# Optimization experiments

Measured on AMD Instinct MI355X. Metric: run time of the kernel, lower is better.

## Reference

```python
import jax, jax.numpy as jnp
import numpy as np

B, T, H, IN, OUT = 128, 256, 1024, 1, 1


def setup_inputs() -> dict:
    key = jax.random.key(0)
    ks = jax.random.split(key, 11)
    s = 1.0 / np.sqrt(H)
    u = lambda k, shape: jax.random.uniform(k, shape, jnp.float32, -s, s)
    return {
        "input_X": jax.random.normal(ks[0], (B, T), jnp.float32),
        "W_ih0": u(ks[1], (4 * H, IN)),
        "W_hh0": u(ks[2], (4 * H, H)),
        "b_ih0": u(ks[3], (4 * H,)),
        "b_hh0": u(ks[4], (4 * H,)),
        "W_ih1": u(ks[5], (4 * H, H)),
        "W_hh1": u(ks[6], (4 * H, H)),
        "b_ih1": u(ks[7], (4 * H,)),
        "b_hh1": u(ks[8], (4 * H,)),
        "W_lin": u(ks[9], (OUT, H)),
        "b_lin": u(ks[10], (OUT,)),
        "future": 0,
    }


def _lstm_cell(x, h, c, W_ih, W_hh, b_ih, b_hh):
    # gates: [B, 4H], PyTorch LSTMCell gate order: i, f, g, o
    gates = x @ W_ih.T + b_ih + h @ W_hh.T + b_hh
    i, f, g, o = jnp.split(gates, 4, axis=-1)
    c_new = jax.nn.sigmoid(f) * c + jax.nn.sigmoid(i) * jnp.tanh(g)
    h_new = jax.nn.sigmoid(o) * jnp.tanh(c_new)
    return h_new, c_new


def reference(input_X, W_ih0, W_hh0, b_ih0, b_hh0, W_ih1, W_hh1, b_ih1, b_hh1,
              W_lin, b_lin, future):
    batch = input_X.shape[0]
    h0 = jnp.zeros((batch, H), input_X.dtype)
    c0 = jnp.zeros((batch, H), input_X.dtype)
    h1 = jnp.zeros((batch, H), input_X.dtype)
    c1 = jnp.zeros((batch, H), input_X.dtype)

    def step(carry, x_t):  # x_t: [B, 1]
        h0, c0, h1, c1 = carry
        h0, c0 = _lstm_cell(x_t, h0, c0, W_ih0, W_hh0, b_ih0, b_hh0)
        h1, c1 = _lstm_cell(h0, h1, c1, W_ih1, W_hh1, b_ih1, b_hh1)
        y = h1 @ W_lin.T + b_lin  # [B, OUT]
        return (h0, c0, h1, c1), y

    xs = input_X.T[:, :, None]  # [T, B, 1]
    carry, ys = jax.lax.scan(step, (h0, c0, h1, c1), xs)
    outputs = jnp.transpose(ys, (1, 0, 2))  # [B, T, OUT]

    y = ys[-1]
    fut = []
    for _ in range(int(future)):
        carry, y = step(carry, y)
        fut.append(y)
    if fut:
        outputs = jnp.concatenate([outputs, jnp.stack(fut, axis=1)], axis=1)
    return jnp.squeeze(outputs, axis=2)  # [B, T+future]
```

## Files before the change

kernel.cpp:

```cpp
#include <hip/hip_runtime.h>
#include <stdint.h>

typedef _Float16 f16;
typedef f16 half8 __attribute__((ext_vector_type(8)));
typedef float f32x4 __attribute__((ext_vector_type(4)));
typedef unsigned long long u64;

constexpr int HID = 1024;
constexpr int NBAT = 128;
constexpr int SEQ = 256;
constexpr int NL0 = 64;
constexpr int NL1 = 128;
constexpr int NBLK = NL0 + NL1;
constexpr int HROWB = 4096;
constexpr int NSLOT = 258;
constexpr size_t SLOTE = (size_t)NBAT * 2048;
constexpr int WROWB0 = 2064;
constexpr int WROWB1 = 4112;
constexpr int ZOFF = 32 * WROWB1;
constexpr int ZBYTES = 4160;
constexpr int WLDS = ZOFF + ZBYTES;
constexpr int LDS_TOTAL = WLDS + 4096;

constexpr int SY_INIT = 0;
constexpr int SY_BARG = 32;
constexpr int SY_CNT = 64;
constexpr int SY_BARAX = 64 + 256;

__device__ __forceinline__ float sigm(float x) { return 1.0f / (1.0f + __expf(-x)); }
__device__ __forceinline__ float tanh_(float x) {
  float e = __expf(2.0f * x);
  return (e - 1.0f) / (e + 1.0f);
}
__device__ __forceinline__ void vm0() {
  asm volatile("s_waitcnt vmcnt(0)" ::: "memory");
}
__device__ __forceinline__ void push8(void* dst, u64 v) {
  (void)__hip_atomic_exchange((u64*)dst, v, __ATOMIC_RELAXED, __HIP_MEMORY_SCOPE_AGENT);
}
__device__ __forceinline__ void spin_until(int* p, int target) {
  uint64_t t0 = __builtin_amdgcn_s_memtime();
  while (__hip_atomic_load(p, __ATOMIC_RELAXED, __HIP_MEMORY_SCOPE_AGENT) < target) {
    __builtin_amdgcn_s_sleep(1);
    if (__builtin_amdgcn_s_memtime() - t0 > (1ULL << 29)) break;
  }
}

__global__ __launch_bounds__(256, 1) void lstm_persist(
    const float* __restrict__ X,
    const float* __restrict__ Wih0, const float* __restrict__ Whh0,
    const float* __restrict__ bih0, const float* __restrict__ bhh0,
    const float* __restrict__ Wih1, const float* __restrict__ Whh1,
    const float* __restrict__ bih1, const float* __restrict__ bhh1,
    const float* __restrict__ Wlin,
    f16* __restrict__ Hbuf,
    float* __restrict__ yp,
    int* __restrict__ sy) {
  extern __shared__ char smem[];
  char* Wl = smem;
  char* Pk = smem + WLDS;

  const int bid = blockIdx.x, tid = threadIdx.x;
  const bool isL0 = bid < NL0;
  const int j = isL0 ? bid : bid - NL0;
  const int w = tid >> 6, l = tid & 63;
  const int l15 = l & 15, lhi = l >> 4;

  int xcd;
  asm volatile("s_getreg_b32 %0, hwreg(HW_REG_XCC_ID)" : "=s"(xcd));
  xcd &= 7;

  if (isL0) {
    for (int it = 0; it < 256; ++it) {
      int e = it * 256 + tid;
      int r = e >> 10, k = e & 1023;
      int grow = (r >> 4) * HID + j * 16 + (r & 15);
      *(f16*)(Wl + r * WROWB0 + 2 * k) = (f16)Whh0[(size_t)grow * HID + k];
    }
  } else {
    for (int it = 0; it < 256; ++it) {
      int e = it * 256 + tid;
      int r = e >> 11, k = e & 2047;
      int grow = (r >> 3) * HID + j * 8 + (r & 7);
      float v = (k < 1024) ? Wih1[(size_t)grow * HID + k]
                           : Whh1[(size_t)grow * HID + (k - 1024)];
      *(f16*)(Wl + r * WROWB1 + 2 * k) = (f16)v;
    }
    for (int e = tid; e < ZBYTES / 2; e += 256)
      *(f16*)(Wl + ZOFF + 2 * e) = (f16)0.f;
  }

  float bi, bf, bg, bo, wi_i = 0, wi_f = 0, wi_g = 0, wi_o = 0, wl = 0;
  if (isL0) {
    int m = j * 16 + l15;
    bi = bih0[m] + bhh0[m];
    bf = bih0[HID + m] + bhh0[HID + m];
    bg = bih0[2 * HID + m] + bhh0[2 * HID + m];
    bo = bih0[3 * HID + m] + bhh0[3 * HID + m];
    wi_i = Wih0[m]; wi_f = Wih0[HID + m];
    wi_g = Wih0[2 * HID + m]; wi_o = Wih0[3 * HID + m];
  } else {
    int u = j * 8 + (l15 & 7);
    bi = bih1[u] + bhh1[u];
    bf = bih1[HID + u] + bhh1[HID + u];
    bg = bih1[2 * HID + u] + bhh1[2 * HID + u];
    bo = bih1[3 * HID + u] + bhh1[3 * HID + u];
    wl = (l15 < 8) ? Wlin[u] : 0.f;
  }
  float cst[8];
#pragma unroll
  for (int q = 0; q < 8; ++q) cst[q] = 0.f;

  int cx = 0, nx = 0;
  if (tid == 0) {
    __hip_atomic_fetch_add(&sy[SY_CNT + 32 * xcd], 1, __ATOMIC_RELAXED,
                           __HIP_MEMORY_SCOPE_AGENT);
    __hip_atomic_fetch_add(&sy[SY_INIT], 1, __ATOMIC_RELAXED, __HIP_MEMORY_SCOPE_AGENT);
    spin_until(&sy[SY_INIT], NBLK);
    cx = __hip_atomic_load(&sy[SY_CNT + 32 * xcd], __ATOMIC_RELAXED,
                           __HIP_MEMORY_SCOPE_AGENT);
#pragma unroll
    for (int x = 0; x < 8; ++x)
      nx += (__hip_atomic_load(&sy[SY_CNT + 32 * x], __ATOMIC_RELAXED,
                               __HIP_MEMORY_SCOPE_AGENT) > 0);
  }
  __syncthreads();

  const char* Wb = Wl + l15 * WROWB0 + lhi * 16;
  const char* Wg0 = Wl + ((l15 < 8) ? (0 * 8 + l15) * WROWB1 : ZOFF) + lhi * 16;
  const char* Wg1 = Wl + ((l15 < 8) ? (1 * 8 + l15) * WROWB1 : ZOFF) + lhi * 16;
  const char* Wg2 = Wl + ((l15 < 8) ? (2 * 8 + l15) * WROWB1 : ZOFF) + lhi * 16;
  const char* Wg3 = Wl + ((l15 < 8) ? (3 * 8 + l15) * WROWB1 : ZOFF) + lhi * 16;

  for (int i = 1; i <= SEQ + 1; ++i) {
    const bool active = isL0 ? (i <= SEQ) : (i >= 2);
    if (active) {
      const char* Asrc = (const char*)(Hbuf + (size_t)(i - 1) * SLOTE);
      char* Hw = (char*)(Hbuf + (size_t)i * SLOTE);
      const char* a0p = Asrc + (size_t)(32 * w + l15) * HROWB + lhi * 16;
      const char* a1p = a0p + (size_t)16 * HROWB;

      if (isL0) {
        float xr[8];
#pragma unroll
        for (int mf = 0; mf < 2; ++mf)
#pragma unroll
          for (int r = 0; r < 4; ++r)
            xr[mf * 4 + r] = X[(32 * w + 16 * mf + 4 * lhi + r) * SEQ + (i - 1)];

        half8 pa[8], pb[8];
#pragma unroll
        for (int k0 = 0; k0 < 8; ++k0) {
          pa[k0] = *(const half8*)(a0p + k0 * 64);
          pb[k0] = *(const half8*)(a1p + k0 * 64);
        }
        f32x4 acc[2][4];
#pragma unroll
        for (int mf = 0; mf < 2; ++mf)
#pragma unroll
          for (int n = 0; n < 4; ++n) acc[mf][n] = f32x4{0.f, 0.f, 0.f, 0.f};

#pragma unroll
        for (int ck = 0; ck < 32; ++ck) {
          half8 a0 = pa[ck & 7], a1 = pb[ck & 7];
          if (ck < 24) {
            pa[ck & 7] = *(const half8*)(a0p + (ck + 8) * 64);
            pb[ck & 7] = *(const half8*)(a1p + (ck + 8) * 64);
          }
          half8 b0 = *(const half8*)(Wb + ck * 64);
          half8 b1 = *(const half8*)(Wb + 16 * WROWB0 + ck * 64);
          half8 b2 = *(const half8*)(Wb + 32 * WROWB0 + ck * 64);
          half8 b3 = *(const half8*)(Wb + 48 * WROWB0 + ck * 64);
          acc[0][0] = __builtin_amdgcn_mfma_f32_16x16x32_f16(a0, b0, acc[0][0], 0, 0, 0);
          acc[0][1] = __builtin_amdgcn_mfma_f32_16x16x32_f16(a0, b1, acc[0][1], 0, 0, 0);
          acc[0][2] = __builtin_amdgcn_mfma_f32_16x16x32_f16(a0, b2, acc[0][2], 0, 0, 0);
          acc[0][3] = __builtin_amdgcn_mfma_f32_16x16x32_f16(a0, b3, acc[0][3], 0, 0, 0);
          acc[1][0] = __builtin_amdgcn_mfma_f32_16x16x32_f16(a1, b0, acc[1][0], 0, 0, 0);
          acc[1][1] = __builtin_amdgcn_mfma_f32_16x16x32_f16(a1, b1, acc[1][1], 0, 0, 0);
          acc[1][2] = __builtin_amdgcn_mfma_f32_16x16x32_f16(a1, b2, acc[1][2], 0, 0, 0);
          acc[1][3] = __builtin_amdgcn_mfma_f32_16x16x32_f16(a1, b3, acc[1][3], 0, 0, 0);
        }

#pragma unroll
        for (int mf = 0; mf < 2; ++mf) {
#pragma unroll
          for (int r = 0; r < 4; ++r) {
            float xv = xr[mf * 4 + r];
            float gi = acc[mf][0][r] + bi + xv * wi_i;
            float gf = acc[mf][1][r] + bf + xv * wi_f;
            float gg = acc[mf][2][r] + bg + xv * wi_g;
            float go = acc[mf][3][r] + bo + xv * wi_o;
            float cn = sigm(gf) * cst[mf * 4 + r] + sigm(gi) * tanh_(gg);
            float hn = sigm(go) * tanh_(cn);
            cst[mf * 4 + r] = cn;
            *(f16*)(Pk + w * 1024 + (16 * mf + 4 * lhi + r) * 32 + l15 * 2) = (f16)hn;
          }
        }
        asm volatile("s_waitcnt lgkmcnt(0)" ::: "memory");
        {
          const char* src = Pk + w * 1024 + (l >> 1) * 32 + (l & 1) * 16;
          u64 v0 = *(const u64*)src;
          u64 v1 = *(const u64*)(src + 8);
          char* dst = Hw + (size_t)(32 * w + (l >> 1)) * HROWB + j * 32 + (l & 1) * 16;
          push8(dst, v0);
          push8(dst + 8, v1);
        }
      } else {
        half8 pa[8], pb[8];
#pragma unroll
        for (int k0 = 0; k0 < 8; ++k0) {
          pa[k0] = *(const half8*)(a0p + k0 * 64);
          pb[k0] = *(const half8*)(a1p + k0 * 64);
        }
        f32x4 acc[2][4];
#pragma unroll
        for (int mf = 0; mf < 2; ++mf)
#pragma unroll
          for (int n = 0; n < 4; ++n) acc[mf][n] = f32x4{0.f, 0.f, 0.f, 0.f};

#pragma unroll
        for (int ck = 0; ck < 64; ++ck) {
          half8 a0 = pa[ck & 7], a1 = pb[ck & 7];
          if (ck < 56) {
            pa[ck & 7] = *(const half8*)(a0p + (ck + 8) * 64);
            pb[ck & 7] = *(const half8*)(a1p + (ck + 8) * 64);
          }
          half8 b0 = *(const half8*)(Wg0 + ck * 64);
          half8 b1 = *(const half8*)(Wg1 + ck * 64);
          half8 b2 = *(const half8*)(Wg2 + ck * 64);
          half8 b3 = *(const half8*)(Wg3 + ck * 64);
          acc[0][0] = __builtin_amdgcn_mfma_f32_16x16x32_f16(a0, b0, acc[0][0], 0, 0, 0);
          acc[0][1] = __builtin_amdgcn_mfma_f32_16x16x32_f16(a0, b1, acc[0][1], 0, 0, 0);
          acc[0][2] = __builtin_amdgcn_mfma_f32_16x16x32_f16(a0, b2, acc[0][2], 0, 0, 0);
          acc[0][3] = __builtin_amdgcn_mfma_f32_16x16x32_f16(a0, b3, acc[0][3], 0, 0, 0);
          acc[1][0] = __builtin_amdgcn_mfma_f32_16x16x32_f16(a1, b0, acc[1][0], 0, 0, 0);
          acc[1][1] = __builtin_amdgcn_mfma_f32_16x16x32_f16(a1, b1, acc[1][1], 0, 0, 0);
          acc[1][2] = __builtin_amdgcn_mfma_f32_16x16x32_f16(a1, b2, acc[1][2], 0, 0, 0);
          acc[1][3] = __builtin_amdgcn_mfma_f32_16x16x32_f16(a1, b3, acc[1][3], 0, 0, 0);
        }

#pragma unroll
        for (int mf = 0; mf < 2; ++mf) {
#pragma unroll
          for (int r = 0; r < 4; ++r) {
            int b = 32 * w + 16 * mf + 4 * lhi + r;
            float gi = acc[mf][0][r] + bi;
            float gf = acc[mf][1][r] + bf;
            float gg = acc[mf][2][r] + bg;
            float go = acc[mf][3][r] + bo;
            float cn = sigm(gf) * cst[mf * 4 + r] + sigm(gi) * tanh_(gg);
            float hn = sigm(go) * tanh_(cn);
            cst[mf * 4 + r] = cn;
            if (l15 < 8)
              *(f16*)(Pk + w * 512 + (16 * mf + 4 * lhi + r) * 16 + l15 * 2) = (f16)hn;
            float v = hn * wl;
            v += __shfl_xor(v, 1);
            v += __shfl_xor(v, 2);
            v += __shfl_xor(v, 4);
            v += __shfl_xor(v, 8);
            if (l15 == 0)
              yp[(size_t)(i - 2) * NBAT * NL1 + b * NL1 + j] = v;
          }
        }
        asm volatile("s_waitcnt lgkmcnt(0)" ::: "memory");
        {
          u64 v = *(const u64*)(Pk + w * 512 + (l >> 1) * 16 + (l & 1) * 8);
          char* dst =
              Hw + (size_t)(32 * w + (l >> 1)) * HROWB + 2048 + j * 16 + (l & 1) * 8;
          push8(dst, v);
        }
      }
    }

    if (i <= SEQ) {
      vm0();
      __syncthreads();
      if (tid == 0) {
        int old = __hip_atomic_fetch_add(&sy[SY_BARAX + 32 * xcd], 1, __ATOMIC_RELAXED,
                                         __HIP_MEMORY_SCOPE_AGENT);
        if (old == cx * i - 1)
          __hip_atomic_fetch_add(&sy[SY_BARG], 1, __ATOMIC_RELAXED,
                                 __HIP_MEMORY_SCOPE_AGENT);
        spin_until(&sy[SY_BARG], nx * i);
      }
      __syncthreads();
    }
  }
}

__global__ __launch_bounds__(256) void zero_ws(f16* Hbuf, int* sy) {
  int g = blockIdx.x * 256 + threadIdx.x, gs = gridDim.x * 256;
  for (size_t idx = g; idx < 2 * SLOTE; idx += gs) Hbuf[idx] = (f16)0.f;
  for (int idx = g; idx < 1024; idx += gs) sy[idx] = 0;
}

__global__ __launch_bounds__(256) void final_kernel(const float* __restrict__ yp,
                                                    const float* __restrict__ blin,
                                                    float* __restrict__ out) {
  const int idx = blockIdx.x * blockDim.x + threadIdx.x;
  const int t = idx >> 7, b = idx & 127;
  const float* p = yp + ((size_t)t * NBAT + b) * NL1;
  float s = 0.f;
#pragma unroll
  for (int q = 0; q < NL1; ++q) s += p[q];
  out[b * SEQ + t] = s + blin[0];
}

extern "C" void kernel_launch(void* const* d_in, const int* in_sizes, int n_in,
                              void* d_out, int out_size, void* d_ws, size_t ws_size,
                              hipStream_t stream) {
  const float* X = (const float*)d_in[0];
  const float* Wih0 = (const float*)d_in[1];
  const float* Whh0 = (const float*)d_in[2];
  const float* bih0 = (const float*)d_in[3];
  const float* bhh0 = (const float*)d_in[4];
  const float* Wih1 = (const float*)d_in[5];
  const float* Whh1 = (const float*)d_in[6];
  const float* bih1 = (const float*)d_in[7];
  const float* bhh1 = (const float*)d_in[8];
  const float* Wlin = (const float*)d_in[9];
  const float* blin = (const float*)d_in[10];
  float* out = (float*)d_out;

  char* p = (char*)d_ws;
  f16* Hbuf = (f16*)p;    p += (size_t)NSLOT * SLOTE * 2;
  float* yp = (float*)p;  p += (size_t)SEQ * NBAT * NL1 * 4;
  int* sy = (int*)p;      p += 1024 * 4;

  hipFuncSetAttribute((const void*)lstm_persist,
                      hipFuncAttributeMaxDynamicSharedMemorySize, LDS_TOTAL);

  zero_ws<<<256, 256, 0, stream>>>(Hbuf, sy);

  lstm_persist<<<NBLK, 256, LDS_TOTAL, stream>>>(
      X, Wih0, Whh0, bih0, bhh0, Wih1, Whh1, bih1, bhh1, Wlin,
      Hbuf, yp, sy);

  final_kernel<<<NBAT, 256, 0, stream>>>(yp, blin, out);
}
```

Before: 4.890 ms.

## Split grid barrier per layer and double waves per block

After: 4.735 ms. 1.03x faster.

```diff
diff --git a/kernel.cpp b/kernel.cpp
--- a/kernel.cpp
+++ b/kernel.cpp
@@ -23,9 +23,12 @@
 constexpr int LDS_TOTAL = WLDS + 4096;
 
 constexpr int SY_INIT = 0;
-constexpr int SY_BARG = 32;
-constexpr int SY_CNT = 64;
-constexpr int SY_BARAX = 64 + 256;
+constexpr int SY_BG0 = 32;
+constexpr int SY_BG1 = 64;
+constexpr int SY_CNT0 = 96;
+constexpr int SY_CNT1 = 96 + 256;
+constexpr int SY_BARX0 = 96 + 512;
+constexpr int SY_BARX1 = 96 + 768;
 
 __device__ __forceinline__ float sigm(float x) { return 1.0f / (1.0f + __expf(-x)); }
 __device__ __forceinline__ float tanh_(float x) {
@@ -46,7 +49,7 @@
   }
 }
 
-__global__ __launch_bounds__(256, 1) void lstm_persist(
+__global__ __launch_bounds__(512, 1) void lstm_persist(
     const float* __restrict__ X,
     const float* __restrict__ Wih0, const float* __restrict__ Whh0,
     const float* __restrict__ bih0, const float* __restrict__ bhh0,
@@ -71,22 +74,22 @@
   xcd &= 7;
 
   if (isL0) {
-    for (int it = 0; it < 256; ++it) {
-      int e = it * 256 + tid;
+    for (int it = 0; it < 128; ++it) {
+      int e = it * 512 + tid;
       int r = e >> 10, k = e & 1023;
       int grow = (r >> 4) * HID + j * 16 + (r & 15);
       *(f16*)(Wl + r * WROWB0 + 2 * k) = (f16)Whh0[(size_t)grow * HID + k];
     }
   } else {
-    for (int it = 0; it < 256; ++it) {
-      int e = it * 256 + tid;
+    for (int it = 0; it < 128; ++it) {
+      int e = it * 512 + tid;
       int r = e >> 11, k = e & 2047;
       int grow = (r >> 3) * HID + j * 8 + (r & 7);
       float v = (k < 1024) ? Wih1[(size_t)grow * HID + k]
                            : Whh1[(size_t)grow * HID + (k - 1024)];
       *(f16*)(Wl + r * WROWB1 + 2 * k) = (f16)v;
     }
-    for (int e = tid; e < ZBYTES / 2; e += 256)
+    for (int e = tid; e < ZBYTES / 2; e += 512)
       *(f16*)(Wl + ZOFF + 2 * e) = (f16)0.f;
   }
 
@@ -107,22 +110,25 @@
     bo = bih1[3 * HID + u] + bhh1[3 * HID + u];
     wl = (l15 < 8) ? Wlin[u] : 0.f;
   }
-  float cst[8];
-#pragma unroll
-  for (int q = 0; q < 8; ++q) cst[q] = 0.f;
-
-  int cx = 0, nx = 0;
+  float cst[4];
+#pragma unroll
+  for (int q = 0; q < 4; ++q) cst[q] = 0.f;
+
+  int cxm = 0, nx0 = 0, nx1 = 0;
   if (tid == 0) {
-    __hip_atomic_fetch_add(&sy[SY_CNT + 32 * xcd], 1, __ATOMIC_RELAXED,
-                           __HIP_MEMORY_SCOPE_AGENT);
+    __hip_atomic_fetch_add(&sy[(isL0 ? SY_CNT0 : SY_CNT1) + 32 * xcd], 1,
+                           __ATOMIC_RELAXED, __HIP_MEMORY_SCOPE_AGENT);
     __hip_atomic_fetch_add(&sy[SY_INIT], 1, __ATOMIC_RELAXED, __HIP_MEMORY_SCOPE_AGENT);
     spin_until(&sy[SY_INIT], NBLK);
-    cx = __hip_atomic_load(&sy[SY_CNT + 32 * xcd], __ATOMIC_RELAXED,
-                           __HIP_MEMORY_SCOPE_AGENT);
-#pragma unroll
-    for (int x = 0; x < 8; ++x)
-      nx += (__hip_atomic_load(&sy[SY_CNT + 32 * x], __ATOMIC_RELAXED,
-                               __HIP_MEMORY_SCOPE_AGENT) > 0);
+    cxm = __hip_atomic_load(&sy[(isL0 ? SY_CNT0 : SY_CNT1) + 32 * xcd],
+                            __ATOMIC_RELAXED, __HIP_MEMORY_SCOPE_AGENT);
+#pragma unroll
+    for (int x = 0; x < 8; ++x) {
+      nx0 += (__hip_atomic_load(&sy[SY_CNT0 + 32 * x], __ATOMIC_RELAXED,
+                                __HIP_MEMORY_SCOPE_AGENT) > 0);
+      nx1 += (__hip_atomic_load(&sy[SY_CNT1 + 32 * x], __ATOMIC_RELAXED,
+                                __HIP_MEMORY_SCOPE_AGENT) > 0);
+    }
   }
   __syncthreads();
 
@@ -133,140 +139,112 @@
   const char* Wg3 = Wl + ((l15 < 8) ? (3 * 8 + l15) * WROWB1 : ZOFF) + lhi * 16;
 
   for (int i = 1; i <= SEQ + 1; ++i) {
+    if (i >= 2) {
+      if (tid == 0) {
+        spin_until(&sy[SY_BG0], nx0 * (i - 1));
+        if (!isL0) spin_until(&sy[SY_BG1], nx1 * (i - 1));
+      }
+      __syncthreads();
+    }
+
     const bool active = isL0 ? (i <= SEQ) : (i >= 2);
     if (active) {
       const char* Asrc = (const char*)(Hbuf + (size_t)(i - 1) * SLOTE);
       char* Hw = (char*)(Hbuf + (size_t)i * SLOTE);
-      const char* a0p = Asrc + (size_t)(32 * w + l15) * HROWB + lhi * 16;
-      const char* a1p = a0p + (size_t)16 * HROWB;
+      const char* a0p = Asrc + (size_t)(16 * w + l15) * HROWB + lhi * 16;
 
       if (isL0) {
-        float xr[8];
-#pragma unroll
-        for (int mf = 0; mf < 2; ++mf)
-#pragma unroll
-          for (int r = 0; r < 4; ++r)
-            xr[mf * 4 + r] = X[(32 * w + 16 * mf + 4 * lhi + r) * SEQ + (i - 1)];
-
-        half8 pa[8], pb[8];
-#pragma unroll
-        for (int k0 = 0; k0 < 8; ++k0) {
-          pa[k0] = *(const half8*)(a0p + k0 * 64);
-          pb[k0] = *(const half8*)(a1p + k0 * 64);
-        }
-        f32x4 acc[2][4];
-#pragma unroll
-        for (int mf = 0; mf < 2; ++mf)
-#pragma unroll
-          for (int n = 0; n < 4; ++n) acc[mf][n] = f32x4{0.f, 0.f, 0.f, 0.f};
+        float xr[4];
+#pragma unroll
+        for (int r = 0; r < 4; ++r)
+          xr[r] = X[(16 * w + 4 * lhi + r) * SEQ + (i - 1)];
+
+        half8 pa[8];
+#pragma unroll
+        for (int k0 = 0; k0 < 8; ++k0) pa[k0] = *(const half8*)(a0p + k0 * 64);
+        f32x4 acc[4];
+#pragma unroll
+        for (int n = 0; n < 4; ++n) acc[n] = f32x4{0.f, 0.f, 0.f, 0.f};
 
 #pragma unroll
         for (int ck = 0; ck < 32; ++ck) {
-          half8 a0 = pa[ck & 7], a1 = pb[ck & 7];
-          if (ck < 24) {
-            pa[ck & 7] = *(const half8*)(a0p + (ck + 8) * 64);
-            pb[ck & 7] = *(const half8*)(a1p + (ck + 8) * 64);
-          }
+          half8 a0 = pa[ck & 7];
+          if (ck < 24) pa[ck & 7] = *(const half8*)(a0p + (ck + 8) * 64);
           half8 b0 = *(const half8*)(Wb + ck * 64);
           half8 b1 = *(const half8*)(Wb + 16 * WROWB0 + ck * 64);
           half8 b2 = *(const half8*)(Wb + 32 * WROWB0 + ck * 64);
           half8 b3 = *(const half8*)(Wb + 48 * WROWB0 + ck * 64);
-          acc[0][0] = __builtin_amdgcn_mfma_f32_16x16x32_f16(a0, b0, acc[0][0], 0, 0, 0);
-          acc[0][1] = __builtin_amdgcn_mfma_f32_16x16x32_f16(a0, b1, acc[0][1], 0, 0, 0);
-          acc[0][2] = __builtin_amdgcn_mfma_f32_16x16x32_f16(a0, b2, acc[0][2], 0, 0, 0);
-          acc[0][3] = __builtin_amdgcn_mfma_f32_16x16x32_f16(a0, b3, acc[0][3], 0, 0, 0);
-          acc[1][0] = __builtin_amdgcn_mfma_f32_16x16x32_f16(a1, b0, acc[1][0], 0, 0, 0);
-          acc[1][1] = __builtin_amdgcn_mfma_f32_16x16x32_f16(a1, b1, acc[1][1], 0, 0, 0);
-          acc[1][2] = __builtin_amdgcn_mfma_f32_16x16x32_f16(a1, b2, acc[1][2], 0, 0, 0);
-          acc[1][3] = __builtin_amdgcn_mfma_f32_16x16x32_f16(a1, b3, acc[1][3], 0, 0, 0);
-        }
-
-#pragma unroll
-        for (int mf = 0; mf < 2; ++mf) {
-#pragma unroll
-          for (int r = 0; r < 4; ++r) {
-            float xv = xr[mf * 4 + r];
-            float gi = acc[mf][0][r] + bi + xv * wi_i;
-            float gf = acc[mf][1][r] + bf + xv * wi_f;
-            float gg = acc[mf][2][r] + bg + xv * wi_g;
-            float go = acc[mf][3][r] + bo + xv * wi_o;
-            float cn = sigm(gf) * cst[mf * 4 + r] + sigm(gi) * tanh_(gg);
-            float hn = sigm(go) * tanh_(cn);
-            cst[mf * 4 + r] = cn;
-            *(f16*)(Pk + w * 1024 + (16 * mf + 4 * lhi + r) * 32 + l15 * 2) = (f16)hn;
-          }
+          acc[0] = __builtin_amdgcn_mfma_f32_16x16x32_f16(a0, b0, acc[0], 0, 0, 0);
+          acc[1] = __builtin_amdgcn_mfma_f32_16x16x32_f16(a0, b1, acc[1], 0, 0, 0);
+          acc[2] = __builtin_amdgcn_mfma_f32_16x16x32_f16(a0, b2, acc[2], 0, 0, 0);
+          acc[3] = __builtin_amdgcn_mfma_f32_16x16x32_f16(a0, b3, acc[3], 0, 0, 0);
+        }
+
+#pragma unroll
+        for (int r = 0; r < 4; ++r) {
+          float xv = xr[r];
+          float gi = acc[0][r] + bi + xv * wi_i;
+          float gf = acc[1][r] + bf + xv * wi_f;
+          float gg = acc[2][r] + bg + xv * wi_g;
+          float go = acc[3][r] + bo + xv * wi_o;
+          float cn = sigm(gf) * cst[r] + sigm(gi) * tanh_(gg);
+          float hn = sigm(go) * tanh_(cn);
+          cst[r] = cn;
+          *(f16*)(Pk + w * 512 + (4 * lhi + r) * 32 + l15 * 2) = (f16)hn;
         }
         asm volatile("s_waitcnt lgkmcnt(0)" ::: "memory");
         {
-          const char* src = Pk + w * 1024 + (l >> 1) * 32 + (l & 1) * 16;
-          u64 v0 = *(const u64*)src;
-          u64 v1 = *(const u64*)(src + 8);
-          char* dst = Hw + (size_t)(32 * w + (l >> 1)) * HROWB + j * 32 + (l & 1) * 16;
-          push8(dst, v0);
-          push8(dst + 8, v1);
+          u64 v = *(const u64*)(Pk + w * 512 + (l >> 2) * 32 + (l & 3) * 8);
+          char* dst = Hw + (size_t)(16 * w + (l >> 2)) * HROWB + j * 32 + (l & 3) * 8;
+          push8(dst, v);
         }
       } else {
-        half8 pa[8], pb[8];
-#pragma unroll
-        for (int k0 = 0; k0 < 8; ++k0) {
-          pa[k0] = *(const half8*)(a0p + k0 * 64);
-          pb[k0] = *(const half8*)(a1p + k0 * 64);
-        }
-        f32x4 acc[2][4];
-#pragma unroll
-        for (int mf = 0; mf < 2; ++mf)
-#pragma unroll
-          for (int n = 0; n < 4; ++n) acc[mf][n] = f32x4{0.f, 0.f, 0.f, 0.f};
+        half8 pa[16];
+#pragma unroll
+        for (int k0 = 0; k0 < 16; ++k0) pa[k0] = *(const half8*)(a0p + k0 * 64);
+        f32x4 acc[4];
+#pragma unroll
+        for (int n = 0; n < 4; ++n) acc[n] = f32x4{0.f, 0.f, 0.f, 0.f};
 
 #pragma unroll
         for (int ck = 0; ck < 64; ++ck) {
-          half8 a0 = pa[ck & 7], a1 = pb[ck & 7];
-          if (ck < 56) {
-            pa[ck & 7] = *(const half8*)(a0p + (ck + 8) * 64);
-            pb[ck & 7] = *(const half8*)(a1p + (ck + 8) * 64);
-          }
+          half8 a0 = pa[ck & 15];
+          if (ck < 48) pa[ck & 15] = *(const half8*)(a0p + (ck + 16) * 64);
           half8 b0 = *(const half8*)(Wg0 + ck * 64);
           half8 b1 = *(const half8*)(Wg1 + ck * 64);
           half8 b2 = *(const half8*)(Wg2 + ck * 64);
           half8 b3 = *(const half8*)(Wg3 + ck * 64);
-          acc[0][0] = __builtin_amdgcn_mfma_f32_16x16x32_f16(a0, b0, acc[0][0], 0, 0, 0);
-          acc[0][1] = __builtin_amdgcn_mfma_f32_16x16x32_f16(a0, b1, acc[0][1], 0, 0, 0);
-          acc[0][2] = __builtin_amdgcn_mfma_f32_16x16x32_f16(a0, b2, acc[0][2], 0, 0, 0);
-          acc[0][3] = __builtin_amdgcn_mfma_f32_16x16x32_f16(a0, b3, acc[0][3], 0, 0, 0);
-          acc[1][0] = __builtin_amdgcn_mfma_f32_16x16x32_f16(a1, b0, acc[1][0], 0, 0, 0);
-          acc[1][1] = __builtin_amdgcn_mfma_f32_16x16x32_f16(a1, b1, acc[1][1], 0, 0, 0);
-          acc[1][2] = __builtin_amdgcn_mfma_f32_16x16x32_f16(a1, b2, acc[1][2], 0, 0, 0);
-          acc[1][3] = __builtin_amdgcn_mfma_f32_16x16x32_f16(a1, b3, acc[1][3], 0, 0, 0);
-        }
-
-#pragma unroll
-        for (int mf = 0; mf < 2; ++mf) {
-#pragma unroll
-          for (int r = 0; r < 4; ++r) {
-            int b = 32 * w + 16 * mf + 4 * lhi + r;
-            float gi = acc[mf][0][r] + bi;
-            float gf = acc[mf][1][r] + bf;
-            float gg = acc[mf][2][r] + bg;
-            float go = acc[mf][3][r] + bo;
-            float cn = sigm(gf) * cst[mf * 4 + r] + sigm(gi) * tanh_(gg);
-            float hn = sigm(go) * tanh_(cn);
-            cst[mf * 4 + r] = cn;
-            if (l15 < 8)
-              *(f16*)(Pk + w * 512 + (16 * mf + 4 * lhi + r) * 16 + l15 * 2) = (f16)hn;
-            float v = hn * wl;
-            v += __shfl_xor(v, 1);
-            v += __shfl_xor(v, 2);
-            v += __shfl_xor(v, 4);
-            v += __shfl_xor(v, 8);
-            if (l15 == 0)
-              yp[(size_t)(i - 2) * NBAT * NL1 + b * NL1 + j] = v;
-          }
+          acc[0] = __builtin_amdgcn_mfma_f32_16x16x32_f16(a0, b0, acc[0], 0, 0, 0);
+          acc[1] = __builtin_amdgcn_mfma_f32_16x16x32_f16(a0, b1, acc[1], 0, 0, 0);
+          acc[2] = __builtin_amdgcn_mfma_f32_16x16x32_f16(a0, b2, acc[2], 0, 0, 0);
+          acc[3] = __builtin_amdgcn_mfma_f32_16x16x32_f16(a0, b3, acc[3], 0, 0, 0);
+        }
+
+#pragma unroll
+        for (int r = 0; r < 4; ++r) {
+          int b = 16 * w + 4 * lhi + r;
+          float gi = acc[0][r] + bi;
+          float gf = acc[1][r] + bf;
+          float gg = acc[2][r] + bg;
+          float go = acc[3][r] + bo;
+          float cn = sigm(gf) * cst[r] + sigm(gi) * tanh_(gg);
+          float hn = sigm(go) * tanh_(cn);
+          cst[r] = cn;
+          if (l15 < 8)
+            *(f16*)(Pk + w * 512 + (4 * lhi + r) * 16 + l15 * 2) = (f16)hn;
+          float v = hn * wl;
+          v += __shfl_xor(v, 1);
+          v += __shfl_xor(v, 2);
+          v += __shfl_xor(v, 4);
+          v += __shfl_xor(v, 8);
+          if (l15 == 0)
+            yp[(size_t)(i - 2) * NBAT * NL1 + b * NL1 + j] = v;
         }
         asm volatile("s_waitcnt lgkmcnt(0)" ::: "memory");
-        {
+        if (l < 32) {
           u64 v = *(const u64*)(Pk + w * 512 + (l >> 1) * 16 + (l & 1) * 8);
           char* dst =
-              Hw + (size_t)(32 * w + (l >> 1)) * HROWB + 2048 + j * 16 + (l & 1) * 8;
+              Hw + (size_t)(16 * w + (l >> 1)) * HROWB + 2048 + j * 16 + (l & 1) * 8;
           push8(dst, v);
         }
       }
@@ -276,14 +254,13 @@
       vm0();
       __syncthreads();
       if (tid == 0) {
-        int old = __hip_atomic_fetch_add(&sy[SY_BARAX + 32 * xcd], 1, __ATOMIC_RELAXED,
+        int* ax = &sy[(isL0 ? SY_BARX0 : SY_BARX1) + 32 * xcd];
+        int old = __hip_atomic_fetch_add(ax, 1, __ATOMIC_RELAXED,
                                          __HIP_MEMORY_SCOPE_AGENT);
-        if (old == cx * i - 1)
-          __hip_atomic_fetch_add(&sy[SY_BARG], 1, __ATOMIC_RELAXED,
+        if (old == cxm * i - 1)
+          __hip_atomic_fetch_add(&sy[isL0 ? SY_BG0 : SY_BG1], 1, __ATOMIC_RELAXED,
                                  __HIP_MEMORY_SCOPE_AGENT);
-        spin_until(&sy[SY_BARG], nx * i);
       }
-      __syncthreads();
     }
   }
 }
@@ -291,7 +268,7 @@
 __global__ __launch_bounds__(256) void zero_ws(f16* Hbuf, int* sy) {
   int g = blockIdx.x * 256 + threadIdx.x, gs = gridDim.x * 256;
   for (size_t idx = g; idx < 2 * SLOTE; idx += gs) Hbuf[idx] = (f16)0.f;
-  for (int idx = g; idx < 1024; idx += gs) sy[idx] = 0;
+  for (int idx = g; idx < 2048; idx += gs) sy[idx] = 0;
 }
 
 __global__ __launch_bounds__(256) void final_kernel(const float* __restrict__ yp,
@@ -325,14 +302,14 @@
   char* p = (char*)d_ws;
   f16* Hbuf = (f16*)p;    p += (size_t)NSLOT * SLOTE * 2;
   float* yp = (float*)p;  p += (size_t)SEQ * NBAT * NL1 * 4;
-  int* sy = (int*)p;      p += 1024 * 4;
+  int* sy = (int*)p;      p += 2048 * 4;
 
   hipFuncSetAttribute((const void*)lstm_persist,
                       hipFuncAttributeMaxDynamicSharedMemorySize, LDS_TOTAL);
 
   zero_ws<<<256, 256, 0, stream>>>(Hbuf, sy);
 
-  lstm_persist<<<NBLK, 256, LDS_TOTAL, stream>>>(
+  lstm_persist<<<NBLK, 512, LDS_TOTAL, stream>>>(
       X, Wih0, Whh0, bih0, bhh0, Wih1, Whh1, bih1, bhh1, Wlin,
       Hbuf, yp, sy);
 
```
